# Performance work log

Measured on AMD Instinct MI355X. Metric: run time of the kernel, lower is better.

The kernel has to match this reference:

```python
import jax, jax.numpy as jnp
import numpy as np

NX = NY = NZ = 192
DX = DY = DZ = 1e-3
DT = 1e-12
EPS0 = 8.8541878128e-12
MU0 = 1.25663706212e-6


def _dcentral(f, axis, inv2d):
    # central difference along `axis`, defined only on the interior of ALL
    # three dims (matches the torch edge lists built for i,j,k in 1..n-2);
    # boundary entries are zero (no scatter contributions there).
    g = jnp.zeros_like(f)
    sp = [slice(1, -1)] * 3
    sm = [slice(1, -1)] * 3
    sp[axis] = slice(2, None)
    sm[axis] = slice(0, -2)
    return g.at[1:-1, 1:-1, 1:-1].set((f[tuple(sp)] - f[tuple(sm)]) * inv2d)


def setup_inputs() -> dict:
    key = jax.random.key(0)
    ks = jax.random.split(key, 9)
    shp = (1, 1, NX, NY, NZ)
    f32 = jnp.float32
    inp = {}
    for name, k in zip(['Ex', 'Ey', 'Ez', 'Hx', 'Hy', 'Hz'], ks[:6]):
        inp[name] = jax.random.normal(k, shp, dtype=f32)
    inp['eps'] = (EPS0 * (1.0 + jax.random.uniform(ks[6], shp))).astype(f32)
    inp['mu'] = (MU0 * (1.0 + jax.random.uniform(ks[7], shp))).astype(f32)
    inp['sigma'] = (1e-3 * jax.random.uniform(ks[8], shp)).astype(f32)
    return inp


def reference(Ex, Ey, Ez, Hx, Hy, Hz, eps, mu, sigma):
    inv2dx = 1.0 / (2.0 * DX)
    inv2dy = 1.0 / (2.0 * DY)
    inv2dz = 1.0 / (2.0 * DZ)
    r3 = lambda a: a.reshape(NX, NY, NZ)  # _flatten3 equivalent layout
    ex, ey, ez = r3(Ex), r3(Ey), r3(Ez)
    hx, hy, hz = r3(Hx), r3(Hy), r3(Hz)
    eps3, mu3, sig3 = r3(eps), r3(mu), r3(sigma)

    # Step 1 (E -> H): H^{n+1/2} = H^{n-1/2} - dt/mu * curl(E^n)
    curlE_x = _dcentral(ez, 1, inv2dy) - _dcentral(ey, 2, inv2dz)
    curlE_y = _dcentral(ex, 2, inv2dz) - _dcentral(ez, 0, inv2dx)
    curlE_z = _dcentral(ey, 0, inv2dx) - _dcentral(ex, 1, inv2dy)
    hx2 = hx - (DT / mu3) * curlE_x
    hy2 = hy - (DT / mu3) * curlE_y
    hz2 = hz - (DT / mu3) * curlE_z

    # Step 2 (H -> E): E^{n+1} = (A-/A+) E^n + dt/(eps A+) * curl(H^{n+1/2})
    A_plus = 1.0 + sig3 * DT / (2.0 * eps3)
    A_minus = 1.0 - sig3 * DT / (2.0 * eps3)
    curlH_x = _dcentral(hz2, 1, inv2dy) - _dcentral(hy2, 2, inv2dz)
    curlH_y = _dcentral(hx2, 2, inv2dz) - _dcentral(hz2, 0, inv2dx)
    curlH_z = _dcentral(hy2, 0, inv2dx) - _dcentral(hx2, 1, inv2dy)
    coefE = A_minus / A_plus
    coefC = DT / (eps3 * A_plus)
    ex2 = coefE * ex + coefC * curlH_x
    ey2 = coefE * ey + coefC * curlH_y
    ez2 = coefE * ez + coefC * curlH_z

    u5 = lambda a: a.reshape(1, 1, NX, NY, NZ)  # _unflatten3
    return (u5(ex2), u5(ey2), u5(ez2), u5(hx2), u5(hy2), u5(hz2))
```

## Files before the change

### kernel.cpp

```cpp
#include <hip/hip_runtime.h>


#define NXD 192
#define NYD 192
#define NZD 192

static constexpr int   N3      = NXD * NYD * NZD;
static constexpr float DTc     = 1e-12f;
static constexpr float INV2D   = 500.0f;

static constexpr int SX = NYD * NZD;
static constexpr int SY = NZD;

__global__ __launch_bounds__(256) void fdtd_step1(
    const float* __restrict__ Ex, const float* __restrict__ Ey, const float* __restrict__ Ez,
    const float* __restrict__ Hx, const float* __restrict__ Hy, const float* __restrict__ Hz,
    const float* __restrict__ mu,
    float* __restrict__ Hx2, float* __restrict__ Hy2, float* __restrict__ Hz2)
{
    int idx = blockIdx.x * blockDim.x + threadIdx.x;
    if (idx >= N3) return;

    int k = idx % NZD;
    int t = idx / NZD;
    int j = t % NYD;
    int i = t / NYD;

    float cx = 0.0f, cy = 0.0f, cz = 0.0f;
    if (i > 0 && i < NXD - 1 && j > 0 && j < NYD - 1 && k > 0 && k < NZD - 1) {
        float dEz_dy = (Ez[idx + SY] - Ez[idx - SY]) * INV2D;
        float dEy_dz = (Ey[idx + 1 ] - Ey[idx - 1 ]) * INV2D;
        float dEx_dz = (Ex[idx + 1 ] - Ex[idx - 1 ]) * INV2D;
        float dEz_dx = (Ez[idx + SX] - Ez[idx - SX]) * INV2D;
        float dEy_dx = (Ey[idx + SX] - Ey[idx - SX]) * INV2D;
        float dEx_dy = (Ex[idx + SY] - Ex[idx - SY]) * INV2D;
        cx = dEz_dy - dEy_dz;
        cy = dEx_dz - dEz_dx;
        cz = dEy_dx - dEx_dy;
    }

    float f = DTc / mu[idx];
    Hx2[idx] = Hx[idx] - f * cx;
    Hy2[idx] = Hy[idx] - f * cy;
    Hz2[idx] = Hz[idx] - f * cz;
}

__global__ __launch_bounds__(256) void fdtd_step2(
    const float* __restrict__ Ex, const float* __restrict__ Ey, const float* __restrict__ Ez,
    const float* __restrict__ Hx2, const float* __restrict__ Hy2, const float* __restrict__ Hz2,
    const float* __restrict__ eps, const float* __restrict__ sigma,
    float* __restrict__ Ex2, float* __restrict__ Ey2, float* __restrict__ Ez2)
{
    int idx = blockIdx.x * blockDim.x + threadIdx.x;
    if (idx >= N3) return;

    int k = idx % NZD;
    int t = idx / NZD;
    int j = t % NYD;
    int i = t / NYD;

    float cx = 0.0f, cy = 0.0f, cz = 0.0f;
    if (i > 0 && i < NXD - 1 && j > 0 && j < NYD - 1 && k > 0 && k < NZD - 1) {
        float dHz_dy = (Hz2[idx + SY] - Hz2[idx - SY]) * INV2D;
        float dHy_dz = (Hy2[idx + 1 ] - Hy2[idx - 1 ]) * INV2D;
        float dHx_dz = (Hx2[idx + 1 ] - Hx2[idx - 1 ]) * INV2D;
        float dHz_dx = (Hz2[idx + SX] - Hz2[idx - SX]) * INV2D;
        float dHy_dx = (Hy2[idx + SX] - Hy2[idx - SX]) * INV2D;
        float dHx_dy = (Hx2[idx + SY] - Hx2[idx - SY]) * INV2D;
        cx = dHz_dy - dHy_dz;
        cy = dHx_dz - dHz_dx;
        cz = dHy_dx - dHx_dy;
    }

    float e  = eps[idx];
    float s  = sigma[idx];
    float half_sdt_over_e = s * DTc / (2.0f * e);
    float Ap = 1.0f + half_sdt_over_e;
    float Am = 1.0f - half_sdt_over_e;
    float coefE = Am / Ap;
    float coefC = DTc / (e * Ap);

    Ex2[idx] = coefE * Ex[idx] + coefC * cx;
    Ey2[idx] = coefE * Ey[idx] + coefC * cy;
    Ez2[idx] = coefE * Ez[idx] + coefC * cz;
}

extern "C" void kernel_launch(void* const* d_in, const int* in_sizes, int n_in,
                              void* d_out, int out_size, void* d_ws, size_t ws_size,
                              hipStream_t stream)
{
    const float* Ex    = (const float*)d_in[0];
    const float* Ey    = (const float*)d_in[1];
    const float* Ez    = (const float*)d_in[2];
    const float* Hx    = (const float*)d_in[3];
    const float* Hy    = (const float*)d_in[4];
    const float* Hz    = (const float*)d_in[5];
    const float* eps   = (const float*)d_in[6];
    const float* mu    = (const float*)d_in[7];
    const float* sigma = (const float*)d_in[8];

    float* out = (float*)d_out;
    float* Ex2 = out + 0 * (size_t)N3;
    float* Ey2 = out + 1 * (size_t)N3;
    float* Ez2 = out + 2 * (size_t)N3;
    float* Hx2 = out + 3 * (size_t)N3;
    float* Hy2 = out + 4 * (size_t)N3;
    float* Hz2 = out + 5 * (size_t)N3;

    const int block = 256;
    const int grid  = (N3 + block - 1) / block;

    fdtd_step1<<<grid, block, 0, stream>>>(Ex, Ey, Ez, Hx, Hy, Hz, mu, Hx2, Hy2, Hz2);
    fdtd_step2<<<grid, block, 0, stream>>>(Ex, Ey, Ez, Hx2, Hy2, Hz2, eps, sigma, Ex2, Ey2, Ez2);
}
```

Measured before the change: 378.1 us.

## Fuse H and E updates into one tiled kernel with shared-memory H halo

Merges the two stencil passes into one kernel. Each block computes the updated H field over its tile plus a one-cell halo into shared memory, then computes the E update from shared memory. This removes the global round trip of H2 between kernels and one launch. The cost is recomputing H on halo cells, about twice the interior volume, plus shared memory use. A block-index swizzle is added to spread neighboring tiles across the grid.

```diff
diff --git a/kernel.cpp b/kernel.cpp
--- a/kernel.cpp
+++ b/kernel.cpp
@@ -5,84 +5,126 @@
 #define NYD 192
 #define NZD 192
 
-static constexpr int   N3      = NXD * NYD * NZD;
-static constexpr float DTc     = 1e-12f;
-static constexpr float INV2D   = 500.0f;
+static constexpr int   N3    = NXD * NYD * NZD;
+static constexpr float DTc   = 1e-12f;
+static constexpr float INV2D = 500.0f;
 
 static constexpr int SX = NYD * NZD;
 static constexpr int SY = NZD;
 
-__global__ __launch_bounds__(256) void fdtd_step1(
+static constexpr int TX = 4, TY = 8, TZ = 32;
+static constexpr int HXT = TX + 2, HYT = TY + 2, HZT = TZ + 2;
+static constexpr int HVOL = HXT * HYT * HZT;
+static constexpr int TVOL = TX * TY * TZ;
+static constexpr int NBX = NXD / TX, NBY = NYD / TY, NBZ = NZD / TZ;
+static constexpr int NBLK = NBX * NBY * NBZ;
+
+__global__ __launch_bounds__(256) void fdtd_fused(
     const float* __restrict__ Ex, const float* __restrict__ Ey, const float* __restrict__ Ez,
     const float* __restrict__ Hx, const float* __restrict__ Hy, const float* __restrict__ Hz,
-    const float* __restrict__ mu,
+    const float* __restrict__ eps, const float* __restrict__ mu, const float* __restrict__ sigma,
+    float* __restrict__ Ex2, float* __restrict__ Ey2, float* __restrict__ Ez2,
     float* __restrict__ Hx2, float* __restrict__ Hy2, float* __restrict__ Hz2)
 {
-    int idx = blockIdx.x * blockDim.x + threadIdx.x;
-    if (idx >= N3) return;
+    __shared__ float sHx[HVOL];
+    __shared__ float sHy[HVOL];
+    __shared__ float sHz[HVOL];
 
-    int k = idx % NZD;
-    int t = idx / NZD;
-    int j = t % NYD;
-    int i = t / NYD;
+    int bid = blockIdx.x;
+    int swz = (bid & 7) * (NBLK / 8) + (bid >> 3);
 
-    float cx = 0.0f, cy = 0.0f, cz = 0.0f;
-    if (i > 0 && i < NXD - 1 && j > 0 && j < NYD - 1 && k > 0 && k < NZD - 1) {
-        float dEz_dy = (Ez[idx + SY] - Ez[idx - SY]) * INV2D;
-        float dEy_dz = (Ey[idx + 1 ] - Ey[idx - 1 ]) * INV2D;
-        float dEx_dz = (Ex[idx + 1 ] - Ex[idx - 1 ]) * INV2D;
-        float dEz_dx = (Ez[idx + SX] - Ez[idx - SX]) * INV2D;
-        float dEy_dx = (Ey[idx + SX] - Ey[idx - SX]) * INV2D;
-        float dEx_dy = (Ex[idx + SY] - Ex[idx - SY]) * INV2D;
-        cx = dEz_dy - dEy_dz;
-        cy = dEx_dz - dEz_dx;
-        cz = dEy_dx - dEx_dy;
+    int bz = swz % NBZ;
+    int t  = swz / NBZ;
+    int by = t % NBY;
+    int bx = t / NBY;
+    int ox = bx * TX, oy = by * TY, oz = bz * TZ;
+
+    int tid = threadIdx.x;
+
+    #pragma unroll
+    for (int it = 0; it < (HVOL + 255) / 256; ++it) {
+        int h = tid + it * 256;
+        if (h < HVOL) {
+            int hz = h % HZT;
+            int tt = h / HZT;
+            int hy = tt % HYT;
+            int hx = tt / HYT;
+            int gi = ox + hx - 1;
+            int gj = oy + hy - 1;
+            int gk = oz + hz - 1;
+
+            float vx = 0.0f, vy = 0.0f, vz = 0.0f;
+            if (gi >= 0 && gi < NXD && gj >= 0 && gj < NYD && gk >= 0 && gk < NZD) {
+                int gidx = (gi * NYD + gj) * NZD + gk;
+                float cx = 0.0f, cy = 0.0f, cz = 0.0f;
+                if (gi > 0 && gi < NXD - 1 && gj > 0 && gj < NYD - 1 && gk > 0 && gk < NZD - 1) {
+                    float dEz_dy = (Ez[gidx + SY] - Ez[gidx - SY]) * INV2D;
+                    float dEy_dz = (Ey[gidx + 1 ] - Ey[gidx - 1 ]) * INV2D;
+                    float dEx_dz = (Ex[gidx + 1 ] - Ex[gidx - 1 ]) * INV2D;
+                    float dEz_dx = (Ez[gidx + SX] - Ez[gidx - SX]) * INV2D;
+                    float dEy_dx = (Ey[gidx + SX] - Ey[gidx - SX]) * INV2D;
+                    float dEx_dy = (Ex[gidx + SY] - Ex[gidx - SY]) * INV2D;
+                    cx = dEz_dy - dEy_dz;
+                    cy = dEx_dz - dEz_dx;
+                    cz = dEy_dx - dEx_dy;
+                }
+                float f = DTc / mu[gidx];
+                vx = Hx[gidx] - f * cx;
+                vy = Hy[gidx] - f * cy;
+                vz = Hz[gidx] - f * cz;
+            }
+            sHx[h] = vx;
+            sHy[h] = vy;
+            sHz[h] = vz;
+        }
     }
 
-    float f = DTc / mu[idx];
-    Hx2[idx] = Hx[idx] - f * cx;
-    Hy2[idx] = Hy[idx] - f * cy;
-    Hz2[idx] = Hz[idx] - f * cz;
-}
+    __syncthreads();
 
-__global__ __launch_bounds__(256) void fdtd_step2(
-    const float* __restrict__ Ex, const float* __restrict__ Ey, const float* __restrict__ Ez,
-    const float* __restrict__ Hx2, const float* __restrict__ Hy2, const float* __restrict__ Hz2,
-    const float* __restrict__ eps, const float* __restrict__ sigma,
-    float* __restrict__ Ex2, float* __restrict__ Ey2, float* __restrict__ Ez2)
-{
-    int idx = blockIdx.x * blockDim.x + threadIdx.x;
-    if (idx >= N3) return;
+    #pragma unroll
+    for (int it = 0; it < TVOL / 256; ++it) {
+        int q  = tid + it * 256;
+        int iz = q % TZ;
+        int tt = q / TZ;
+        int iy = tt % TY;
+        int ix = tt / TY;
+        int gi = ox + ix, gj = oy + iy, gk = oz + iz;
+        int gidx = (gi * NYD + gj) * NZD + gk;
 
-    int k = idx % NZD;
-    int t = idx / NZD;
-    int j = t % NYD;
-    int i = t / NYD;
+        int l = ((ix + 1) * HYT + (iy + 1)) * HZT + (iz + 1);
 
-    float cx = 0.0f, cy = 0.0f, cz = 0.0f;
-    if (i > 0 && i < NXD - 1 && j > 0 && j < NYD - 1 && k > 0 && k < NZD - 1) {
-        float dHz_dy = (Hz2[idx + SY] - Hz2[idx - SY]) * INV2D;
-        float dHy_dz = (Hy2[idx + 1 ] - Hy2[idx - 1 ]) * INV2D;
-        float dHx_dz = (Hx2[idx + 1 ] - Hx2[idx - 1 ]) * INV2D;
-        float dHz_dx = (Hz2[idx + SX] - Hz2[idx - SX]) * INV2D;
-        float dHy_dx = (Hy2[idx + SX] - Hy2[idx - SX]) * INV2D;
-        float dHx_dy = (Hx2[idx + SY] - Hx2[idx - SY]) * INV2D;
-        cx = dHz_dy - dHy_dz;
-        cy = dHx_dz - dHz_dx;
-        cz = dHy_dx - dHx_dy;
+        float hx2 = sHx[l];
+        float hy2 = sHy[l];
+        float hz2 = sHz[l];
+        Hx2[gidx] = hx2;
+        Hy2[gidx] = hy2;
+        Hz2[gidx] = hz2;
+
+        float cx = 0.0f, cy = 0.0f, cz = 0.0f;
+        if (gi > 0 && gi < NXD - 1 && gj > 0 && gj < NYD - 1 && gk > 0 && gk < NZD - 1) {
+            float dHz_dy = (sHz[l + HZT]       - sHz[l - HZT])       * INV2D;
+            float dHy_dz = (sHy[l + 1]         - sHy[l - 1])         * INV2D;
+            float dHx_dz = (sHx[l + 1]         - sHx[l - 1])         * INV2D;
+            float dHz_dx = (sHz[l + HYT * HZT] - sHz[l - HYT * HZT]) * INV2D;
+            float dHy_dx = (sHy[l + HYT * HZT] - sHy[l - HYT * HZT]) * INV2D;
+            float dHx_dy = (sHx[l + HZT]       - sHx[l - HZT])       * INV2D;
+            cx = dHz_dy - dHy_dz;
+            cy = dHx_dz - dHz_dx;
+            cz = dHy_dx - dHx_dy;
+        }
+
+        float e = eps[gidx];
+        float s = sigma[gidx];
+        float half_sdt_over_e = s * DTc / (2.0f * e);
+        float Ap = 1.0f + half_sdt_over_e;
+        float Am = 1.0f - half_sdt_over_e;
+        float coefE = Am / Ap;
+        float coefC = DTc / (e * Ap);
+
+        Ex2[gidx] = coefE * Ex[gidx] + coefC * cx;
+        Ey2[gidx] = coefE * Ey[gidx] + coefC * cy;
+        Ez2[gidx] = coefE * Ez[gidx] + coefC * cz;
     }
-
-    float e  = eps[idx];
-    float s  = sigma[idx];
-    float half_sdt_over_e = s * DTc / (2.0f * e);
-    float Ap = 1.0f + half_sdt_over_e;
-    float Am = 1.0f - half_sdt_over_e;
-    float coefE = Am / Ap;
-    float coefC = DTc / (e * Ap);
-
-    Ex2[idx] = coefE * Ex[idx] + coefC * cx;
-    Ey2[idx] = coefE * Ey[idx] + coefC * cy;
-    Ez2[idx] = coefE * Ez[idx] + coefC * cz;
 }
 
 extern "C" void kernel_launch(void* const* d_in, const int* in_sizes, int n_in,
@@ -107,9 +149,6 @@
     float* Hy2 = out + 4 * (size_t)N3;
     float* Hz2 = out + 5 * (size_t)N3;
 
-    const int block = 256;
-    const int grid  = (N3 + block - 1) / block;
-
-    fdtd_step1<<<grid, block, 0, stream>>>(Ex, Ey, Ez, Hx, Hy, Hz, mu, Hx2, Hy2, Hz2);
-    fdtd_step2<<<grid, block, 0, stream>>>(Ex, Ey, Ez, Hx2, Hy2, Hz2, eps, sigma, Ex2, Ey2, Ez2);
+    fdtd_fused<<<NBLK, 256, 0, stream>>>(Ex, Ey, Ez, Hx, Hy, Hz, eps, mu, sigma,
+                                         Ex2, Ey2, Ez2, Hx2, Hy2, Hz2);
 }
```

Result: slower. 461.7 us (+22.1%).
